# Performance work log

Hardware: AMD Instinct MI355X
Metric: run time of the kernel (lower is better)

The kernel has to match this reference:

```python
import jax, jax.numpy as jnp
import numpy as np

HEAD_DIM = 64
NUM_HEADS = 32
ROPE_BASE = 10000.0


def _rope_interleaved(x):
    # x: [B, T, H, D]; interleaved RoPE on query, seqlen_offset = 0
    B, T, H, D = x.shape
    inv_freq = 1.0 / (ROPE_BASE ** (jnp.arange(0, D, 2, dtype=jnp.float32) / D))  # [D/2]
    t = jnp.arange(T, dtype=jnp.float32)
    freqs = t[:, None] * inv_freq[None, :]          # [T, D/2]
    cos = jnp.cos(freqs)[None, :, None, :]          # [1, T, 1, D/2]
    sin = jnp.sin(freqs)[None, :, None, :]
    x1 = x[..., 0::2]
    x2 = x[..., 1::2]
    o1 = x1 * cos - x2 * sin
    o2 = x1 * sin + x2 * cos
    out = jnp.stack([o1, o2], axis=-1).reshape(x.shape)  # re-interleave
    return out


def setup_inputs() -> dict:
    key = jax.random.key(0)
    k1, k2, k3, k4, k5 = jax.random.split(key, 5)
    B, T, Dm = 2, 2048, 2048
    H, Dh = NUM_HEADS, HEAD_DIM
    scale = 0.02
    return {
        "hidden_states": jax.random.normal(k1, (B, T, Dm), jnp.float32),
        "shared_k": jax.random.normal(k2, (B, T, H, Dh), jnp.float32),
        "shared_v": jax.random.normal(k3, (B, T, H, Dh), jnp.float32),
        "Wq": jax.random.normal(k4, (Dm, Dm), jnp.float32) * scale,
        "Wo": jax.random.normal(k5, (Dm, Dm), jnp.float32) * scale,
    }


def reference(hidden_states, shared_k, shared_v, Wq, Wo):
    B, T, Dm = hidden_states.shape
    H, Dh = NUM_HEADS, HEAD_DIM
    # q projection (nn.Linear: x @ W.T)
    q = (hidden_states @ Wq.T).reshape(B, T, H, Dh)
    # rotary on q only (seqlen_offset = shared_k_len - q_len = 0)
    q = _rope_interleaved(q)
    # parallel causal attention over shared KV cache (window_size=None)
    scale = 1.0 / jnp.sqrt(jnp.asarray(Dh, jnp.float32))
    scores = jnp.einsum('bqhd,bkhd->bhqk', q, shared_k) * scale
    causal = jnp.tril(jnp.ones((T, T), dtype=bool))
    scores = jnp.where(causal[None, None], scores, -jnp.inf)
    p = jax.nn.softmax(scores, axis=-1)
    o = jnp.einsum('bhqk,bkhd->bqhd', p, shared_v)
    o = o.reshape(B, T, Dm)
    return o @ Wo.T
```

## Files before the change

kernel.cpp:

```cpp
#include <hip/hip_runtime.h>
#include <stdint.h>

typedef short short8 __attribute__((ext_vector_type(8)));
typedef float f32x4 __attribute__((ext_vector_type(4)));
typedef int int2v __attribute__((ext_vector_type(2)));
typedef int int4v __attribute__((ext_vector_type(4)));

#define QSCALE 0.1803368801111137f
#define FREQC 0.4152410118609203f

__device__ __forceinline__ float bf2f(unsigned short u) {
    union { unsigned int i; float f; } x; x.i = ((unsigned int)u) << 16; return x.f;
}
__device__ __forceinline__ unsigned short f2bf(float f) {
    union { float f; unsigned int i; } x; x.f = f;
    unsigned int i = x.i;
    unsigned int r = i + 0x7FFFu + ((i >> 16) & 1u);
    return (unsigned short)(r >> 16);
}
__device__ __forceinline__ int cvtpk_bf16(float lo, float hi) {
    int r;
    asm("v_cvt_pk_bf16_f32 %0, %1, %2" : "=v"(r) : "v"(lo), "v"(hi));
    return r;
}

#define GLDS16(g, l) \
    __builtin_amdgcn_global_load_lds((const __attribute__((address_space(1))) void*)(g), \
                                     (__attribute__((address_space(3))) void*)(l), 16, 0, 0)

#define WAITVM(n) asm volatile("s_waitcnt vmcnt(" #n ")" ::: "memory")

__global__ __launch_bounds__(256) void cvt_tr(
    const float* __restrict__ hs, const float* __restrict__ k,
    const float* __restrict__ wq, const float* __restrict__ wo,
    const float* __restrict__ V,
    unsigned short* __restrict__ hs_b, unsigned short* __restrict__ k_b,
    unsigned short* __restrict__ wq_b, unsigned short* __restrict__ wo_b,
    unsigned short* __restrict__ Vt) {
    __shared__ float s[64 * 65];
    int blk = blockIdx.x;
    int tid = threadIdx.x;
    if (blk < 24576) {
        const float* in; unsigned short* out; int i;
        if (blk < 8192)        { in = hs; out = hs_b; i = blk * 256 + tid; }
        else if (blk < 16384)  { in = k;  out = k_b;  i = (blk - 8192) * 256 + tid; }
        else if (blk < 20480)  { in = wq; out = wq_b; i = (blk - 16384) * 256 + tid; }
        else                   { in = wo; out = wo_b; i = (blk - 20480) * 256 + tid; }
        float4 v = ((const float4*)in)[i];
        ushort4 o;
        o.x = f2bf(v.x); o.y = f2bf(v.y); o.z = f2bf(v.z); o.w = f2bf(v.w);
        ((ushort4*)out)[i] = o;
        return;
    }
    int tb = blk - 24576;
    int t0 = (tb & 31) * 64;
    int bh = tb >> 5;
    int b = bh >> 5, h = bh & 31;
#pragma unroll
    for (int it = 0; it < 4; ++it) {
        int c = tid + it * 256;
        int t = c >> 4;
        int d0 = (c & 15) * 4;
        float4 v = *(const float4*)(V + (size_t)(((b * 2048 + t0 + t) * 32 + h)) * 64 + d0);
        s[t * 65 + d0 + 0] = v.x; s[t * 65 + d0 + 1] = v.y;
        s[t * 65 + d0 + 2] = v.z; s[t * 65 + d0 + 3] = v.w;
    }
    __syncthreads();
#pragma unroll
    for (int it = 0; it < 2; ++it) {
        int c = tid + it * 256;
        int d = c >> 3;
        int tt = (c & 7) * 8;
        short8 pk;
#pragma unroll
        for (int j = 0; j < 8; ++j) pk[j] = (short)f2bf(s[(tt + j) * 65 + d]);
        *(short8*)(Vt + (size_t)(bh * 64 + d) * 2048 + t0 + tt) = pk;
    }
}

template <bool BF16_OUT>
__global__ __launch_bounds__(256) void gemm_bt(
    const unsigned short* __restrict__ A,
    const unsigned short* __restrict__ B,
    void* __restrict__ Cout,
    int M, int N, int K)
{
    __shared__ __align__(16) unsigned short lA[2][128 * 64];
    __shared__ __align__(16) unsigned short lB[2][128 * 64];
    int tid = threadIdx.x, lane = tid & 63, wave = tid >> 6;
    int wm = (wave >> 1) * 64, wn = (wave & 1) * 64;
    int m16 = lane & 15, q = lane >> 4;
    int rowBase = blockIdx.x * 128, colBase = blockIdx.y * 128;
    f32x4 acc[4][4] = {};

    int sr = lane >> 3;
    int g  = (lane & 7) ^ sr;
    const unsigned short* gAp = A + (size_t)(rowBase + wave * 32 + sr) * K + g * 8;
    const unsigned short* gBp = B + (size_t)(colBase + wave * 32 + sr) * K + g * 8;

#define GSTAGE(buf, k0)                                                                   \
    do {                                                                                  \
        _Pragma("unroll")                                                                 \
        for (int i = 0; i < 4; ++i) {                                                     \
            GLDS16(gAp + (size_t)(8 * i) * K + (k0), &lA[buf][(wave * 32 + 8 * i) * 64]); \
            GLDS16(gBp + (size_t)(8 * i) * K + (k0), &lB[buf][(wave * 32 + 8 * i) * 64]); \
        }                                                                                 \
    } while (0)

    GSTAGE(0, 0);
    WAITVM(0);
    __builtin_amdgcn_s_barrier();
    int cur = 0;
    for (int k0 = 0; k0 < K; k0 += 64) {
        if (k0 + 64 < K) {
            GSTAGE(cur ^ 1, k0 + 64);
            WAITVM(8);
        } else {
            WAITVM(0);
        }
        __builtin_amdgcn_s_barrier();
        const unsigned short* la = lA[cur];
        const unsigned short* lb = lB[cur];
#pragma unroll
        for (int kk = 0; kk < 2; ++kk) {
            short8 af[4], bfr[4];
#pragma unroll
            for (int i = 0; i < 4; ++i) {
                int RA = wm + i * 16 + m16;
                af[i]  = *(const short8*)&la[RA * 64 + (((kk * 4 + q) ^ (RA & 7)) * 8)];
                int RB = wn + i * 16 + m16;
                bfr[i] = *(const short8*)&lb[RB * 64 + (((kk * 4 + q) ^ (RB & 7)) * 8)];
            }
#pragma unroll
            for (int i = 0; i < 4; ++i)
#pragma unroll
                for (int jn = 0; jn < 4; ++jn)
                    acc[i][jn] = __builtin_amdgcn_mfma_f32_16x16x32_bf16(af[i], bfr[jn], acc[i][jn], 0, 0, 0);
        }
        __builtin_amdgcn_s_barrier();
        cur ^= 1;
    }
#pragma unroll
    for (int i = 0; i < 4; ++i)
#pragma unroll
        for (int jn = 0; jn < 4; ++jn)
#pragma unroll
            for (int r = 0; r < 4; ++r) {
                int row = rowBase + wm + i * 16 + q * 4 + r;
                int col = colBase + wn + jn * 16 + m16;
                float v = acc[i][jn][r];
                if (BF16_OUT) ((unsigned short*)Cout)[(size_t)row * N + col] = f2bf(v);
                else          ((float*)Cout)[(size_t)row * N + col] = v;
            }
}

__global__ __launch_bounds__(256, 4) void attn(
    const unsigned short* __restrict__ Q,
    const unsigned short* __restrict__ Kb,
    const unsigned short* __restrict__ Vt,
    unsigned short* __restrict__ O)
{
    __shared__ __align__(16) unsigned short sK[2][64 * 64];
    __shared__ __align__(16) unsigned short sV[2][64 * 64];
    int tid = threadIdx.x, lane = tid & 63, w = tid >> 6;
    int m16 = lane & 15, q = lane >> 4;
    int rx = m16 & 7;
    int flat = blockIdx.x;
    int bh = flat & 63, p = flat >> 6;
    int b = bh >> 5, h = bh & 31;
    int qtA = 31 - p, qtB = p;

    short8 aqA0, aqA1, aqB0, aqB1;
    {
        int tA = qtA * 64 + w * 16 + m16;
        int tB = qtB * 64 + w * 16 + m16;
        const unsigned short* rowA = Q + (size_t)(b * 2048 + tA) * 2048 + h * 64 + q * 8;
        const unsigned short* rowB = Q + (size_t)(b * 2048 + tB) * 2048 + h * 64 + q * 8;
        short8 a0 = *(const short8*)rowA, a1 = *(const short8*)(rowA + 32);
        short8 b0 = *(const short8*)rowB, b1 = *(const short8*)(rowB + 32);
        float tfA = (float)tA, tfB = (float)tB;
#pragma unroll
        for (int j = 0; j < 4; ++j) {
            float inv0 = __builtin_amdgcn_exp2f(-FREQC * (float)(q * 4 + j));
            float inv1 = __builtin_amdgcn_exp2f(-FREQC * (float)(16 + q * 4 + j));
            float cA0 = __cosf(tfA * inv0), sA0 = __sinf(tfA * inv0);
            float cA1 = __cosf(tfA * inv1), sA1 = __sinf(tfA * inv1);
            float cB0 = __cosf(tfB * inv0), sB0 = __sinf(tfB * inv0);
            float cB1 = __cosf(tfB * inv1), sB1 = __sinf(tfB * inv1);
            float x1, x2;
            x1 = bf2f((unsigned short)a0[2 * j]); x2 = bf2f((unsigned short)a0[2 * j + 1]);
            aqA0[2 * j]     = (short)f2bf((x1 * cA0 - x2 * sA0) * QSCALE);
            aqA0[2 * j + 1] = (short)f2bf((x1 * sA0 + x2 * cA0) * QSCALE);
            x1 = bf2f((unsigned short)a1[2 * j]); x2 = bf2f((unsigned short)a1[2 * j + 1]);
            aqA1[2 * j]     = (short)f2bf((x1 * cA1 - x2 * sA1) * QSCALE);
            aqA1[2 * j + 1] = (short)f2bf((x1 * sA1 + x2 * cA1) * QSCALE);
            x1 = bf2f((unsigned short)b0[2 * j]); x2 = bf2f((unsigned short)b0[2 * j + 1]);
            aqB0[2 * j]     = (short)f2bf((x1 * cB0 - x2 * sB0) * QSCALE);
            aqB0[2 * j + 1] = (short)f2bf((x1 * sB0 + x2 * cB0) * QSCALE);
            x1 = bf2f((unsigned short)b1[2 * j]); x2 = bf2f((unsigned short)b1[2 * j + 1]);
            aqB1[2 * j]     = (short)f2bf((x1 * cB1 - x2 * sB1) * QSCALE);
            aqB1[2 * j + 1] = (short)f2bf((x1 * sB1 + x2 * cB1) * QSCALE);
        }
    }

    float lrunA = 0.f, lrunB = 0.f;
    f32x4 accOA[4], accOB[4];
#pragma unroll
    for (int nt = 0; nt < 4; ++nt) {
        f32x4 z = {0.f, 0.f, 0.f, 0.f};
        accOA[nt] = z; accOB[nt] = z;
    }

    int sr = lane >> 3, g = (lane & 7) ^ sr;
    int rb = w * 16;
    const unsigned short* kgp = Kb + (size_t)(b * 2048 + rb + sr) * 2048 + h * 64 + g * 8;
    const unsigned short* vgp = Vt + (size_t)((b * 32 + h) * 64 + rb + sr) * 2048 + g * 8;

#define ASTAGE(kt, bi)                                                              \
    do {                                                                            \
        int kb0 = (kt) * 64;                                                        \
        _Pragma("unroll")                                                           \
        for (int i = 0; i < 2; ++i) {                                               \
            GLDS16(kgp + (size_t)(kb0 + 8 * i) * 2048, &sK[bi][(rb + 8 * i) * 64]); \
            GLDS16(vgp + (size_t)(8 * i) * 2048 + kb0, &sV[bi][(rb + 8 * i) * 64]); \
        }                                                                           \
    } while (0)

    ASTAGE(0, 0);
    WAITVM(0);
    __builtin_amdgcn_s_barrier();
    int cur = 0;
    for (int kt = 0; kt <= qtA; ++kt) {
        if (kt < qtA) {
            ASTAGE(kt + 1, cur ^ 1);
            WAITVM(4);
        } else {
            WAITVM(0);
        }
        __builtin_amdgcn_s_barrier();
        bool doB = (kt <= qtB);
        bool diagA = (kt == qtA), diagB = (kt == qtB);
        const unsigned short* kbuf = sK[cur];
        const unsigned short* vbuf = sV[cur];

        int pkA[4][2], pkB[4][2];
#pragma unroll
        for (int nt = 0; nt < 4; ++nt) {
            const unsigned short* kr = kbuf + (nt * 16 + m16) * 64;
            short8 bk0 = *(const short8*)&kr[(q ^ rx) * 8];
            short8 bk1 = *(const short8*)&kr[((4 + q) ^ rx) * 8];
            f32x4 zA = {0.f, 0.f, 0.f, 0.f};
            zA = __builtin_amdgcn_mfma_f32_16x16x32_bf16(bk0, aqA0, zA, 0, 0, 0);
            zA = __builtin_amdgcn_mfma_f32_16x16x32_bf16(bk1, aqA1, zA, 0, 0, 0);
            float e[4];
#pragma unroll
            for (int r = 0; r < 4; ++r) {
                float s = zA[r];
                if (diagA && (nt * 16 + q * 4 + r > w * 16 + m16)) s = -__builtin_inff();
                e[r] = __builtin_amdgcn_exp2f(s);
            }
            lrunA += (e[0] + e[1]) + (e[2] + e[3]);
            pkA[nt][0] = cvtpk_bf16(e[0], e[1]);
            pkA[nt][1] = cvtpk_bf16(e[2], e[3]);
            if (doB) {
                f32x4 zB = {0.f, 0.f, 0.f, 0.f};
                zB = __builtin_amdgcn_mfma_f32_16x16x32_bf16(bk0, aqB0, zB, 0, 0, 0);
                zB = __builtin_amdgcn_mfma_f32_16x16x32_bf16(bk1, aqB1, zB, 0, 0, 0);
                float eb[4];
#pragma unroll
                for (int r = 0; r < 4; ++r) {
                    float s = zB[r];
                    if (diagB && (nt * 16 + q * 4 + r > w * 16 + m16)) s = -__builtin_inff();
                    eb[r] = __builtin_amdgcn_exp2f(s);
                }
                lrunB += (eb[0] + eb[1]) + (eb[2] + eb[3]);
                pkB[nt][0] = cvtpk_bf16(eb[0], eb[1]);
                pkB[nt][1] = cvtpk_bf16(eb[2], eb[3]);
            }
        }

        int4v tA0 = {pkA[0][0], pkA[0][1], pkA[1][0], pkA[1][1]};
        int4v tA1 = {pkA[2][0], pkA[2][1], pkA[3][0], pkA[3][1]};
        short8 apA0 = __builtin_bit_cast(short8, tA0);
        short8 apA1 = __builtin_bit_cast(short8, tA1);
        short8 apB0, apB1;
        if (doB) {
            int4v tB0 = {pkB[0][0], pkB[0][1], pkB[1][0], pkB[1][1]};
            int4v tB1 = {pkB[2][0], pkB[2][1], pkB[3][0], pkB[3][1]};
            apB0 = __builtin_bit_cast(short8, tB0);
            apB1 = __builtin_bit_cast(short8, tB1);
        }

#pragma unroll
        for (int nt = 0; nt < 4; ++nt) {
            const unsigned short* vr = vbuf + (nt * 16 + m16) * 64;
            int2v a0 = *(const int2v*)&vr[(((q >> 1) + 0) ^ rx) * 8 + (q & 1) * 4];
            int2v a1 = *(const int2v*)&vr[(((q >> 1) + 2) ^ rx) * 8 + (q & 1) * 4];
            int2v a2 = *(const int2v*)&vr[(((q >> 1) + 4) ^ rx) * 8 + (q & 1) * 4];
            int2v a3 = *(const int2v*)&vr[(((q >> 1) + 6) ^ rx) * 8 + (q & 1) * 4];
            int4v tv0 = {a0.x, a0.y, a1.x, a1.y};
            int4v tv1 = {a2.x, a2.y, a3.x, a3.y};
            short8 bv0 = __builtin_bit_cast(short8, tv0);
            short8 bv1 = __builtin_bit_cast(short8, tv1);
            accOA[nt] = __builtin_amdgcn_mfma_f32_16x16x32_bf16(apA0, bv0, accOA[nt], 0, 0, 0);
            accOA[nt] = __builtin_amdgcn_mfma_f32_16x16x32_bf16(apA1, bv1, accOA[nt], 0, 0, 0);
            if (doB) {
                accOB[nt] = __builtin_amdgcn_mfma_f32_16x16x32_bf16(apB0, bv0, accOB[nt], 0, 0, 0);
                accOB[nt] = __builtin_amdgcn_mfma_f32_16x16x32_bf16(apB1, bv1, accOB[nt], 0, 0, 0);
            }
        }
        __builtin_amdgcn_s_barrier();
        cur ^= 1;
    }

    lrunA += __shfl_xor(lrunA, 16); lrunA += __shfl_xor(lrunA, 32);
    lrunB += __shfl_xor(lrunB, 16); lrunB += __shfl_xor(lrunB, 32);
    float invA = 1.0f / lrunA, invB = 1.0f / lrunB;
    float nA[4], nB[4];
#pragma unroll
    for (int r = 0; r < 4; ++r) {
        nA[r] = __shfl(invA, q * 4 + r);
        nB[r] = __shfl(invB, q * 4 + r);
    }
#pragma unroll
    for (int nt = 0; nt < 4; ++nt)
#pragma unroll
        for (int r = 0; r < 4; ++r) {
            int col = h * 64 + nt * 16 + m16;
            O[(size_t)(b * 2048 + qtA * 64 + w * 16 + q * 4 + r) * 2048 + col] =
                f2bf(accOA[nt][r] * nA[r]);
            O[(size_t)(b * 2048 + qtB * 64 + w * 16 + q * 4 + r) * 2048 + col] =
                f2bf(accOB[nt][r] * nB[r]);
        }
}

extern "C" void kernel_launch(void* const* d_in, const int* in_sizes, int n_in,
                              void* d_out, int out_size, void* d_ws, size_t ws_size,
                              hipStream_t stream) {
    const float* hs = (const float*)d_in[0];
    const float* sk = (const float*)d_in[1];
    const float* sv = (const float*)d_in[2];
    const float* wq = (const float*)d_in[3];
    const float* wo = (const float*)d_in[4];
    float* out = (float*)d_out;

    char* ws = (char*)d_ws;
    unsigned short* hid_b = (unsigned short*)(ws);
    unsigned short* wq_b  = (unsigned short*)(ws + ((size_t)16 << 20));
    unsigned short* wo_b  = (unsigned short*)(ws + ((size_t)24 << 20));
    unsigned short* k_b   = (unsigned short*)(ws + ((size_t)32 << 20));
    unsigned short* vt_b  = (unsigned short*)(ws + ((size_t)48 << 20));
    unsigned short* q_b   = (unsigned short*)(ws + ((size_t)64 << 20));
    unsigned short* o_b   = (unsigned short*)(ws + ((size_t)80 << 20));

    cvt_tr<<<26624, 256, 0, stream>>>(hs, sk, wq, wo, sv, hid_b, k_b, wq_b, wo_b, vt_b);
    gemm_bt<true><<<dim3(32, 16), 256, 0, stream>>>(hid_b, wq_b, (void*)q_b, 4096, 2048, 2048);
    attn<<<1024, 256, 0, stream>>>(q_b, k_b, vt_b, o_b);
    gemm_bt<false><<<dim3(32, 16), 256, 0, stream>>>(o_b, wo_b, (void*)out, 4096, 2048, 2048);
}
```

Baseline: 285.5 us.

## Use 256x128 GEMM tiles with 8 waves and triple-buffered loads; widen conversion

```diff
diff --git a/kernel.cpp b/kernel.cpp
--- a/kernel.cpp
+++ b/kernel.cpp
@@ -40,19 +40,24 @@
     __shared__ float s[64 * 65];
     int blk = blockIdx.x;
     int tid = threadIdx.x;
-    if (blk < 24576) {
+    if (blk < 12288) {
         const float* in; unsigned short* out; int i;
-        if (blk < 8192)        { in = hs; out = hs_b; i = blk * 256 + tid; }
-        else if (blk < 16384)  { in = k;  out = k_b;  i = (blk - 8192) * 256 + tid; }
-        else if (blk < 20480)  { in = wq; out = wq_b; i = (blk - 16384) * 256 + tid; }
-        else                   { in = wo; out = wo_b; i = (blk - 20480) * 256 + tid; }
-        float4 v = ((const float4*)in)[i];
-        ushort4 o;
-        o.x = f2bf(v.x); o.y = f2bf(v.y); o.z = f2bf(v.z); o.w = f2bf(v.w);
-        ((ushort4*)out)[i] = o;
+        if (blk < 4096)        { in = hs; out = hs_b; i = blk; }
+        else if (blk < 8192)   { in = k;  out = k_b;  i = blk - 4096; }
+        else if (blk < 10240)  { in = wq; out = wq_b; i = blk - 8192; }
+        else                   { in = wo; out = wo_b; i = blk - 10240; }
+        size_t base = ((size_t)i * 256 + tid) * 8;
+        float4 v0 = *(const float4*)(in + base);
+        float4 v1 = *(const float4*)(in + base + 4);
+        short8 o;
+        o[0] = (short)f2bf(v0.x); o[1] = (short)f2bf(v0.y);
+        o[2] = (short)f2bf(v0.z); o[3] = (short)f2bf(v0.w);
+        o[4] = (short)f2bf(v1.x); o[5] = (short)f2bf(v1.y);
+        o[6] = (short)f2bf(v1.z); o[7] = (short)f2bf(v1.w);
+        *(short8*)(out + base) = o;
         return;
     }
-    int tb = blk - 24576;
+    int tb = blk - 12288;
     int t0 = (tb & 31) * 64;
     int bh = tb >> 5;
     int b = bh >> 5, h = bh & 31;
@@ -79,66 +84,68 @@
 }
 
 template <bool BF16_OUT>
-__global__ __launch_bounds__(256) void gemm_bt(
+__global__ __launch_bounds__(512, 2) void gemm_bt(
     const unsigned short* __restrict__ A,
     const unsigned short* __restrict__ B,
     void* __restrict__ Cout,
     int M, int N, int K)
 {
-    __shared__ __align__(16) unsigned short lA[2][128 * 64];
-    __shared__ __align__(16) unsigned short lB[2][128 * 64];
+    __shared__ __align__(16) unsigned short lA[3][256 * 64];
+    __shared__ __align__(16) unsigned short lB[3][128 * 64];
     int tid = threadIdx.x, lane = tid & 63, wave = tid >> 6;
     int wm = (wave >> 1) * 64, wn = (wave & 1) * 64;
     int m16 = lane & 15, q = lane >> 4;
-    int rowBase = blockIdx.x * 128, colBase = blockIdx.y * 128;
+    int rowBase = blockIdx.x * 256, colBase = blockIdx.y * 128;
     f32x4 acc[4][4] = {};
 
     int sr = lane >> 3;
     int g  = (lane & 7) ^ sr;
     const unsigned short* gAp = A + (size_t)(rowBase + wave * 32 + sr) * K + g * 8;
-    const unsigned short* gBp = B + (size_t)(colBase + wave * 32 + sr) * K + g * 8;
-
-#define GSTAGE(buf, k0)                                                                   \
-    do {                                                                                  \
-        _Pragma("unroll")                                                                 \
-        for (int i = 0; i < 4; ++i) {                                                     \
-            GLDS16(gAp + (size_t)(8 * i) * K + (k0), &lA[buf][(wave * 32 + 8 * i) * 64]); \
-            GLDS16(gBp + (size_t)(8 * i) * K + (k0), &lB[buf][(wave * 32 + 8 * i) * 64]); \
-        }                                                                                 \
+    const unsigned short* gBp = B + (size_t)(colBase + wave * 16 + sr) * K + g * 8;
+
+#define GSTAGE(buf, k0)                                                                     \
+    do {                                                                                    \
+        _Pragma("unroll")                                                                   \
+        for (int gi = 0; gi < 4; ++gi)                                                      \
+            GLDS16(gAp + (size_t)(8 * gi) * K + (k0), &lA[buf][(wave * 32 + 8 * gi) * 64]); \
+        _Pragma("unroll")                                                                   \
+        for (int gi = 0; gi < 2; ++gi)                                                      \
+            GLDS16(gBp + (size_t)(8 * gi) * K + (k0), &lB[buf][(wave * 16 + 8 * gi) * 64]); \
     } while (0)
 
     GSTAGE(0, 0);
-    WAITVM(0);
+    GSTAGE(1, 64);
+    WAITVM(6);
     __builtin_amdgcn_s_barrier();
-    int cur = 0;
-    for (int k0 = 0; k0 < K; k0 += 64) {
-        if (k0 + 64 < K) {
-            GSTAGE(cur ^ 1, k0 + 64);
-            WAITVM(8);
-        } else {
-            WAITVM(0);
-        }
+    int cur = 0, nxt = 2;
+    const int NT = 32;
+    for (int i = 0; i < NT; ++i) {
+        if (i < NT - 2) GSTAGE(nxt, (i + 2) * 64);
+        if (i < NT - 2)      WAITVM(12);
+        else if (i == NT - 2) WAITVM(6);
+        else                  WAITVM(0);
         __builtin_amdgcn_s_barrier();
-        const unsigned short* la = lA[cur];
-        const unsigned short* lb = lB[cur];
+        const unsigned short* la = &lA[cur][0];
+        const unsigned short* lb = &lB[cur][0];
 #pragma unroll
         for (int kk = 0; kk < 2; ++kk) {
             short8 af[4], bfr[4];
 #pragma unroll
-            for (int i = 0; i < 4; ++i) {
-                int RA = wm + i * 16 + m16;
-                af[i]  = *(const short8*)&la[RA * 64 + (((kk * 4 + q) ^ (RA & 7)) * 8)];
-                int RB = wn + i * 16 + m16;
-                bfr[i] = *(const short8*)&lb[RB * 64 + (((kk * 4 + q) ^ (RB & 7)) * 8)];
-            }
-#pragma unroll
-            for (int i = 0; i < 4; ++i)
+            for (int i2 = 0; i2 < 4; ++i2) {
+                int RA = wm + i2 * 16 + m16;
+                af[i2]  = *(const short8*)&la[RA * 64 + (((kk * 4 + q) ^ (RA & 7)) * 8)];
+                int RB = wn + i2 * 16 + m16;
+                bfr[i2] = *(const short8*)&lb[RB * 64 + (((kk * 4 + q) ^ (RB & 7)) * 8)];
+            }
+#pragma unroll
+            for (int i2 = 0; i2 < 4; ++i2)
 #pragma unroll
                 for (int jn = 0; jn < 4; ++jn)
-                    acc[i][jn] = __builtin_amdgcn_mfma_f32_16x16x32_bf16(af[i], bfr[jn], acc[i][jn], 0, 0, 0);
+                    acc[i2][jn] = __builtin_amdgcn_mfma_f32_16x16x32_bf16(af[i2], bfr[jn], acc[i2][jn], 0, 0, 0);
         }
         __builtin_amdgcn_s_barrier();
-        cur ^= 1;
+        cur = (cur == 2) ? 0 : cur + 1;
+        nxt = (nxt == 2) ? 0 : nxt + 1;
     }
 #pragma unroll
     for (int i = 0; i < 4; ++i)
@@ -216,14 +223,14 @@
     const unsigned short* kgp = Kb + (size_t)(b * 2048 + rb + sr) * 2048 + h * 64 + g * 8;
     const unsigned short* vgp = Vt + (size_t)((b * 32 + h) * 64 + rb + sr) * 2048 + g * 8;
 
-#define ASTAGE(kt, bi)                                                              \
-    do {                                                                            \
-        int kb0 = (kt) * 64;                                                        \
-        _Pragma("unroll")                                                           \
-        for (int i = 0; i < 2; ++i) {                                               \
-            GLDS16(kgp + (size_t)(kb0 + 8 * i) * 2048, &sK[bi][(rb + 8 * i) * 64]); \
-            GLDS16(vgp + (size_t)(8 * i) * 2048 + kb0, &sV[bi][(rb + 8 * i) * 64]); \
-        }                                                                           \
+#define ASTAGE(kt, bi)                                                               \
+    do {                                                                             \
+        int kb0 = (kt) * 64;                                                         \
+        _Pragma("unroll")                                                            \
+        for (int gi = 0; gi < 2; ++gi) {                                             \
+            GLDS16(kgp + (size_t)(kb0 + 8 * gi) * 2048, &sK[bi][(rb + 8 * gi) * 64]); \
+            GLDS16(vgp + (size_t)(8 * gi) * 2048 + kb0, &sV[bi][(rb + 8 * gi) * 64]); \
+        }                                                                            \
     } while (0)
 
     ASTAGE(0, 0);
@@ -353,8 +360,8 @@
     unsigned short* q_b   = (unsigned short*)(ws + ((size_t)64 << 20));
     unsigned short* o_b   = (unsigned short*)(ws + ((size_t)80 << 20));
 
-    cvt_tr<<<26624, 256, 0, stream>>>(hs, sk, wq, wo, sv, hid_b, k_b, wq_b, wo_b, vt_b);
-    gemm_bt<true><<<dim3(32, 16), 256, 0, stream>>>(hid_b, wq_b, (void*)q_b, 4096, 2048, 2048);
+    cvt_tr<<<14336, 256, 0, stream>>>(hs, sk, wq, wo, sv, hid_b, k_b, wq_b, wo_b, vt_b);
+    gemm_bt<true><<<dim3(16, 16), 512, 0, stream>>>(hid_b, wq_b, (void*)q_b, 4096, 2048, 2048);
     attn<<<1024, 256, 0, stream>>>(q_b, k_b, vt_b, o_b);
-    gemm_bt<false><<<dim3(32, 16), 256, 0, stream>>>(o_b, wo_b, (void*)out, 4096, 2048, 2048);
-}
+    gemm_bt<false><<<dim3(16, 16), 512, 0, stream>>>(o_b, wo_b, (void*)out, 4096, 2048, 2048);
+}
```

Result: slower. 293.4 us (+2.7%).
